# Kernel tuning notes

Hardware: AMD Instinct MI355X
Metric: run time of the kernel (lower is better)

Reference implementation:

```python
import jax, jax.numpy as jnp
import numpy as np

N_GROUPS = 32  # getGroupSize(.) assumed -> channels // 8 (or //24 for 3*ch) == 32 for ch=256
HEADS = 4


def group_norm(x, gamma, beta, groups=N_GROUPS, eps=1e-5):
    n, c = x.shape
    xg = x.reshape(n, groups, c // groups)
    mu = xg.mean(-1, keepdims=True)
    var = xg.var(-1, keepdims=True)
    xn = ((xg - mu) * jax.lax.rsqrt(var + eps)).reshape(n, c)
    return xn * gamma + beta


def setup_inputs():
    key = jax.random.key(0)
    N, E, CH, HID = 2000, 16000, 256, 256
    ks = jax.random.split(key, 24)

    def w(k, shape, s=0.02):
        return (jax.random.normal(k, shape) * s).astype(jnp.float32)

    inp = {
        'x': jax.random.normal(ks[0], (N, CH), jnp.float32),
        'edge_index': jax.random.randint(ks[1], (2, E), 0, N),
        'edge_attr': jax.random.normal(ks[2], (E, CH), jnp.float32),
        # edge_mlp: GN(3ch)+ReLU -> Linear(3ch,hid) -> GN(hid)+ReLU -> Linear(hid,ch)
        'gn_e1_g': jnp.ones((3 * CH,), jnp.float32), 'gn_e1_b': jnp.zeros((3 * CH,), jnp.float32),
        'We1': w(ks[3], (3 * CH, HID)), 'be1': jnp.zeros((HID,), jnp.float32),
        'gn_e2_g': jnp.ones((HID,), jnp.float32), 'gn_e2_b': jnp.zeros((HID,), jnp.float32),
        'We2': w(ks[4], (HID, CH)), 'be2': jnp.zeros((CH,), jnp.float32),
        # actN: GN(ch)+ReLU
        'gn_n_g': jnp.ones((CH,), jnp.float32), 'gn_n_b': jnp.zeros((CH,), jnp.float32),
        # multi-head attention projections
        'Wq': w(ks[5], (CH, CH)), 'bq': jnp.zeros((CH,), jnp.float32),
        'Wk': w(ks[6], (CH, CH)), 'bk': jnp.zeros((CH,), jnp.float32),
        'Wv': w(ks[7], (CH, CH)), 'bv': jnp.zeros((CH,), jnp.float32),
        'Wo': w(ks[8], (CH, CH)), 'bo': jnp.zeros((CH,), jnp.float32),
        # node_mlp: Linear(2ch,hid) -> GN(hid)+ReLU -> Linear(hid,ch)
        'Wn1': w(ks[9], (2 * CH, HID)), 'bn1': jnp.zeros((HID,), jnp.float32),
        'gn_n2_g': jnp.ones((HID,), jnp.float32), 'gn_n2_b': jnp.zeros((HID,), jnp.float32),
        'Wn2': w(ks[10], (HID, CH)), 'bn2': jnp.zeros((CH,), jnp.float32),
    }
    return inp


def reference(x, edge_index, edge_attr,
              gn_e1_g, gn_e1_b, We1, be1, gn_e2_g, gn_e2_b, We2, be2,
              gn_n_g, gn_n_b, Wq, bq, Wk, bk, Wv, bv, Wo, bo,
              Wn1, bn1, gn_n2_g, gn_n2_b, Wn2, bn2):
    row, col = edge_index[0], edge_index[1]
    N, ch = x.shape
    E = edge_attr.shape[0]
    dk = ch // HEADS

    # ---- edge model: cat(src, tgt, e) -> GN/ReLU -> Lin -> GN/ReLU -> Lin (+res) ----
    e_in = jnp.concatenate([x[row], x[col], edge_attr], axis=1)  # [E, 3ch]
    h = jax.nn.relu(group_norm(e_in, gn_e1_g, gn_e1_b))
    h = h @ We1 + be1
    h = jax.nn.relu(group_norm(h, gn_e2_g, gn_e2_b))
    e_out = h @ We2 + be2 + edge_attr  # [E, ch]

    # ---- node model: dense-masked MHA, queries=nodes, keys/values=edges ----
    mask = jnp.zeros((N, E), x.dtype).at[col, jnp.arange(E)].set(1.0)  # scatter adjacency
    q = (x @ Wq + bq).reshape(N, HEADS, dk)
    k = (e_out @ Wk + bk).reshape(E, HEADS, dk)
    v = (e_out @ Wv + bv).reshape(E, HEADS, dk)
    scores = jnp.einsum('nhd,ehd->hne', q, k) / jnp.sqrt(jnp.float32(dk))  # [H, N, E]
    scores = jnp.where(mask[None] > 0, scores, jnp.float32(-1e9))
    attn = jax.nn.softmax(scores, axis=-1)
    g = jnp.einsum('hne,ehd->nhd', attn, v).reshape(N, ch) @ Wo + bo  # [N, ch]

    xa = jax.nn.relu(group_norm(x, gn_n_g, gn_n_b))
    h = jnp.concatenate([xa, g], axis=1) @ Wn1 + bn1  # thinker='cat'
    h = jax.nn.relu(group_norm(h, gn_n2_g, gn_n2_b))
    n_out = h @ Wn2 + bn2 + x  # residual

    return n_out, e_out
```

## Files before the change

kernel.cpp:

```cpp
#include <hip/hip_runtime.h>
#include <hip/hip_bf16.h>
#include <stdint.h>
#include <math.h>

#define CH 256

typedef __attribute__((ext_vector_type(8)))  short short8;
typedef __attribute__((ext_vector_type(16))) short short16;
typedef __attribute__((ext_vector_type(4)))  float f32x4;

#define GL2LDS16(g, l) __builtin_amdgcn_global_load_lds(                       \
    (const __attribute__((address_space(1))) void*)(g),                        \
    (__attribute__((address_space(3))) void*)(l), 16, 0, 0)

__device__ inline short f2bf(float f) {
    __hip_bfloat16 h = __float2bfloat16(f);
    short s;
    __builtin_memcpy(&s, &h, 2);
    return s;
}

__device__ inline float bf2f(short s) {
    unsigned u = ((unsigned)(unsigned short)s) << 16;
    float f;
    __builtin_memcpy(&f, &u, 4);
    return f;
}

__device__ inline float warp_sum64(float v) {
    v += __shfl_xor(v, 32, 64);
    v += __shfl_xor(v, 16, 64);
    v += __shfl_xor(v, 8, 64);
    v += __shfl_xor(v, 4, 64);
    v += __shfl_xor(v, 2, 64);
    v += __shfl_xor(v, 1, 64);
    return v;
}

__device__ inline float warp_max64(float v) {
    v = fmaxf(v, __shfl_xor(v, 32, 64));
    v = fmaxf(v, __shfl_xor(v, 16, 64));
    v = fmaxf(v, __shfl_xor(v, 8, 64));
    v = fmaxf(v, __shfl_xor(v, 4, 64));
    v = fmaxf(v, __shfl_xor(v, 2, 64));
    v = fmaxf(v, __shfl_xor(v, 1, 64));
    return v;
}

struct GArgs {
    const short* A; const short* Bt; const float* bias; const float* res;
    float* C; short* Cbf;
    const float* gamma; const float* beta; float* vbar;
    int M, K, Nc, ldc, coff;
    const short* A2; const short* Bt2; const float* bias2; short* Cbf2;
    int M2, Nc2, y_split;
    const short* xbf; const short* eabf; const int* rowi; const int* coli;
    const float* mu; const float* rs; const float* vg; const float* vbt;
};

template <int BM, int BN, int AMODE, int EPI, int DUAL, int VB>
__global__ __launch_bounds__(256) void mfma_gemm(GArgs g)
{
    constexpr int BK = 64;
    constexpr int AK = AMODE ? (BK + 8) : BK;
    constexpr int HM = BM / 2, HN = BN / 2;
    constexpr int FM = HM / 16, FN = HN / 16;
    constexpr int PA = BM / 32;
    constexpr int PB = BN / 32;
    __shared__ short As[BM * AK];
    __shared__ short Bs[BN * BK];
    __shared__ int sidx[AMODE ? 2 * BM : 1];

    const short* A = g.A; const short* Bt = g.Bt;
    const float* bias = g.bias; const float* res = g.res;
    float* C = g.C; short* Cbf = g.Cbf;
    int M = g.M, ldc = g.ldc, co = g.coff;
    const int K = g.K;
    int by = blockIdx.y, bx = blockIdx.x;
    bool qrole = false;
    if constexpr (DUAL) {
        if (by >= g.y_split) {
            by -= g.y_split;
            if (bx * BN >= g.Nc2) return;
            qrole = true;
            A = g.A2; Bt = g.Bt2; bias = g.bias2; Cbf = g.Cbf2;
            C = nullptr; res = nullptr;
            M = g.M2; ldc = g.Nc2; co = 0;
        }
    }

    const int t = threadIdx.x;
    const int wave = t >> 6, lane = t & 63;
    const int q = lane >> 4, l16 = lane & 15;
    const int row0 = by * BM;
    const int col0 = bx * BN;
    const int wm = wave & 1, wn = wave >> 1;

    if constexpr (AMODE) {
        if (t < BM) {
            int gr = row0 + t; if (gr >= M) gr = M - 1;
            sidx[t] = g.rowi[gr];
            sidx[BM + t] = g.coli[gr];
        }
        __syncthreads();
    }

    f32x4 acc[FM][FN];
    #pragma unroll
    for (int i = 0; i < FM; i++)
        #pragma unroll
        for (int j = 0; j < FN; j++) acc[i][j] = (f32x4){0.f, 0.f, 0.f, 0.f};

    for (int k0 = 0; k0 < K; k0 += BK) {
        if constexpr (AMODE == 1) {
            int reg = k0 >> 8;
            int rloc = t >> 3;
            int c8 = (t & 7) * 8;
            int pos = k0 + c8;
            int G = pos / 24;
            float4 ga  = *(const float4*)&g.vg[pos];
            float4 ga2 = *(const float4*)&g.vg[pos + 4];
            float4 gb  = *(const float4*)&g.vbt[pos];
            float4 gb2 = *(const float4*)&g.vbt[pos + 4];
            int off = pos & 255;
            #pragma unroll
            for (int p = 0; p < BM / 32; p++) {
                int r2 = p * 32 + rloc;
                int e = row0 + r2; if (e >= M) e = M - 1;
                const short* srow;
                if (reg == 0)      srow = g.xbf + (size_t)sidx[r2] * CH;
                else if (reg == 1) srow = g.xbf + (size_t)sidx[BM + r2] * CH;
                else               srow = g.eabf + (size_t)e * CH;
                short8 v8 = *(const short8*)&srow[off];
                float mm = g.mu[(size_t)e * 32 + G];
                float rr = g.rs[(size_t)e * 32 + G];
                short8 o;
                o[0] = f2bf(fmaxf((bf2f(v8[0]) - mm) * rr * ga.x + gb.x, 0.f));
                o[1] = f2bf(fmaxf((bf2f(v8[1]) - mm) * rr * ga.y + gb.y, 0.f));
                o[2] = f2bf(fmaxf((bf2f(v8[2]) - mm) * rr * ga.z + gb.z, 0.f));
                o[3] = f2bf(fmaxf((bf2f(v8[3]) - mm) * rr * ga.w + gb.w, 0.f));
                o[4] = f2bf(fmaxf((bf2f(v8[4]) - mm) * rr * ga2.x + gb2.x, 0.f));
                o[5] = f2bf(fmaxf((bf2f(v8[5]) - mm) * rr * ga2.y + gb2.y, 0.f));
                o[6] = f2bf(fmaxf((bf2f(v8[6]) - mm) * rr * ga2.z + gb2.z, 0.f));
                o[7] = f2bf(fmaxf((bf2f(v8[7]) - mm) * rr * ga2.w + gb2.w, 0.f));
                *(short8*)&As[r2 * AK + c8] = o;
            }
        } else {
            #pragma unroll
            for (int p = 0; p < PA; p++) {
                int chunk = p * 256 + t;
                int r = chunk >> 3;
                int cs = (((chunk & 7) ^ (r & 7)) * 8);
                int gr = row0 + r; if (gr >= M) gr = M - 1;
                const short* gsrc = A + (size_t)gr * K + k0 + cs;
                short* ldst = &As[(p * 256 + wave * 64) * 8];
                GL2LDS16(gsrc, ldst);
            }
        }
        #pragma unroll
        for (int p = 0; p < PB; p++) {
            int chunk = p * 256 + t;
            int r = chunk >> 3;
            int cs = (((chunk & 7) ^ (r & 7)) * 8);
            const short* gsrc = Bt + (size_t)(col0 + r) * K + k0 + cs;
            short* ldst = &Bs[(p * 256 + wave * 64) * 8];
            GL2LDS16(gsrc, ldst);
        }
        __syncthreads();
        #pragma unroll
        for (int ks = 0; ks < 2; ks++) {
            short8 af[FM], bf[FN];
            #pragma unroll
            for (int mi = 0; mi < FM; mi++) {
                int R = wm * HM + mi * 16 + l16;
                if constexpr (AMODE == 1)
                    af[mi] = *(const short8*)&As[R * AK + ks * 32 + q * 8];
                else {
                    int slot = ((ks * 4 + q) ^ (R & 7)) * 8;
                    af[mi] = *(const short8*)&As[R * BK + slot];
                }
            }
            #pragma unroll
            for (int ni = 0; ni < FN; ni++) {
                int R = wn * HN + ni * 16 + l16;
                int slot = ((ks * 4 + q) ^ (R & 7)) * 8;
                bf[ni] = *(const short8*)&Bs[R * BK + slot];
            }
            #pragma unroll
            for (int mi = 0; mi < FM; mi++)
                #pragma unroll
                for (int ni = 0; ni < FN; ni++)
                    acc[mi][ni] = __builtin_amdgcn_mfma_f32_16x16x32_bf16(
                        af[mi], bf[ni], acc[mi][ni], 0, 0, 0);
        }
        __syncthreads();
    }

    #pragma unroll
    for (int ni = 0; ni < FN; ni++) {
        int cg = col0 + wn * HN + ni * 16 + l16;
        float bv = bias[cg];
        if constexpr (EPI == 1) {
            float ga = g.gamma[cg], be = g.beta[cg];
            #pragma unroll
            for (int mi = 0; mi < FM; mi++) {
                #pragma unroll
                for (int r = 0; r < 4; r++) {
                    float v = acc[mi][ni][r] + bv;
                    float s = v, sq = v * v;
                    s += __shfl_xor(s, 1, 64);  sq += __shfl_xor(sq, 1, 64);
                    s += __shfl_xor(s, 2, 64);  sq += __shfl_xor(sq, 2, 64);
                    s += __shfl_xor(s, 4, 64);  sq += __shfl_xor(sq, 4, 64);
                    float mean = s * 0.125f;
                    float var = sq * 0.125f - mean * mean;
                    float o = fmaxf((v - mean) * rsqrtf(var + 1e-5f) * ga + be, 0.f);
                    int rg = row0 + wm * HM + mi * 16 + q * 4 + r;
                    if (rg < M) Cbf[(size_t)rg * ldc + co + cg] = f2bf(o);
                }
            }
        } else {
            #pragma unroll
            for (int mi = 0; mi < FM; mi++) {
                #pragma unroll
                for (int r = 0; r < 4; r++) {
                    int rg = row0 + wm * HM + mi * 16 + q * 4 + r;
                    if (rg < M) {
                        float v = acc[mi][ni][r] + bv;
                        if (res) v += res[(size_t)rg * ldc + co + cg];
                        if (C)   C[(size_t)rg * ldc + co + cg] = v;
                        if (Cbf) Cbf[(size_t)rg * ldc + co + cg] = f2bf(v);
                    }
                }
            }
            if constexpr (VB) {
                if (!qrole && cg >= 256) {
                    float part = 0.f;
                    #pragma unroll
                    for (int mi = 0; mi < FM; mi++)
                        #pragma unroll
                        for (int r = 0; r < 4; r++) {
                            int rg = row0 + wm * HM + mi * 16 + q * 4 + r;
                            if (rg < M) part += acc[mi][ni][r] + bv;
                        }
                    part += __shfl_xor(part, 16, 64);
                    part += __shfl_xor(part, 32, 64);
                    if (q == 0) atomicAdd(&g.vbar[cg - 256], part);
                }
            }
        }
    }
}

struct PrepPack {
    const float* wsrc[8];
    short* wdst[8];
    int wK[8];
    int wstart[8];
    int NW, NP;
    const float* x;
    short* x_bf;
    short* cat_bf;
    float2* xs;
    const float* gng;
    const float* gnb;
    float* vbar;
    const float* bk;
    const float* bv;
    float* bkv;
    int* counts;
    int N;
};

__global__ __launch_bounds__(256) void prep_kernel(PrepPack p)
{
    int bid = blockIdx.x;
    int t = threadIdx.x;
    if (bid < p.NW) {
        int m = 0;
        #pragma unroll
        for (int i = 1; i < 8; i++) if (bid >= p.wstart[i]) m = i;
        int k0 = (bid - p.wstart[m]) * 16;
        const float* src = p.wsrc[m];
        short16 o;
        #pragma unroll
        for (int j = 0; j < 16; j++) o[j] = f2bf(src[(size_t)(k0 + j) * 256 + t]);
        *(short16*)(p.wdst[m] + (size_t)t * p.wK[m] + k0) = o;
        return;
    }
    if (bid >= p.NW + p.NP) {
        int i = (bid - p.NW - p.NP) * 256 + t;
        if (i < p.N) p.counts[i] = 0;
        return;
    }
    int pb = bid - p.NW;
    if (pb == 0) {
        p.vbar[t] = 0.f;
        p.bkv[t] = p.bk[t];
        p.bkv[256 + t] = p.bv[t];
    }
    int r = pb * 8 + (t >> 5);
    int g = t & 31;
    if (r >= p.N) return;
    size_t xb = (size_t)r * CH + g * 8;
    float4 a = *(const float4*)&p.x[xb];
    float4 b = *(const float4*)&p.x[xb + 4];
    short8 xr;
    xr[0] = f2bf(a.x); xr[1] = f2bf(a.y); xr[2] = f2bf(a.z); xr[3] = f2bf(a.w);
    xr[4] = f2bf(b.x); xr[5] = f2bf(b.y); xr[6] = f2bf(b.z); xr[7] = f2bf(b.w);
    *(short8*)&p.x_bf[xb] = xr;
    float s  = a.x + a.y + a.z + a.w + b.x + b.y + b.z + b.w;
    float s2 = a.x*a.x + a.y*a.y + a.z*a.z + a.w*a.w
             + b.x*b.x + b.y*b.y + b.z*b.z + b.w*b.w;
    p.xs[(size_t)r * 32 + g] = make_float2(s, s2);
    float m = s * 0.125f;
    float var = s2 * 0.125f - m * m;
    float rsd = rsqrtf(var + 1e-5f);
    float4 g0 = *(const float4*)&p.gng[g * 8];
    float4 g1 = *(const float4*)&p.gng[g * 8 + 4];
    float4 b0 = *(const float4*)&p.gnb[g * 8];
    float4 b1 = *(const float4*)&p.gnb[g * 8 + 4];
    short8 o;
    o[0] = f2bf(fmaxf((a.x - m) * rsd * g0.x + b0.x, 0.f));
    o[1] = f2bf(fmaxf((a.y - m) * rsd * g0.y + b0.y, 0.f));
    o[2] = f2bf(fmaxf((a.z - m) * rsd * g0.z + b0.z, 0.f));
    o[3] = f2bf(fmaxf((a.w - m) * rsd * g0.w + b0.w, 0.f));
    o[4] = f2bf(fmaxf((b.x - m) * rsd * g1.x + b1.x, 0.f));
    o[5] = f2bf(fmaxf((b.y - m) * rsd * g1.y + b1.y, 0.f));
    o[6] = f2bf(fmaxf((b.z - m) * rsd * g1.z + b1.z, 0.f));
    o[7] = f2bf(fmaxf((b.w - m) * rsd * g1.w + b1.w, 0.f));
    *(short8*)&p.cat_bf[(size_t)r * (2 * CH) + g * 8] = o;
}

__global__ __launch_bounds__(256) void estats_kernel(
    const float* __restrict__ eattr, const int* __restrict__ rowi,
    const int* __restrict__ coli, const float2* __restrict__ xs,
    float* __restrict__ mu, float* __restrict__ rs,
    short* __restrict__ eabf, int* __restrict__ counts, int E)
{
    __shared__ float2 ea[8][32];
    int t = threadIdx.x;
    int slot = t >> 5, g = t & 31;
    int e = blockIdx.x * 8 + slot;
    float4 a = *(const float4*)&eattr[(size_t)e * CH + g * 8];
    float4 b = *(const float4*)&eattr[(size_t)e * CH + g * 8 + 4];
    short8 o8;
    o8[0] = f2bf(a.x); o8[1] = f2bf(a.y); o8[2] = f2bf(a.z); o8[3] = f2bf(a.w);
    o8[4] = f2bf(b.x); o8[5] = f2bf(b.y); o8[6] = f2bf(b.z); o8[7] = f2bf(b.w);
    *(short8*)&eabf[(size_t)e * CH + g * 8] = o8;
    float s  = a.x + a.y + a.z + a.w + b.x + b.y + b.z + b.w;
    float s2 = a.x*a.x + a.y*a.y + a.z*a.z + a.w*a.w
             + b.x*b.x + b.y*b.y + b.z*b.z + b.w*b.w;
    ea[slot][g] = make_float2(s, s2);
    int r = rowi[e], c = coli[e];
    if (g == 0) atomicAdd(&counts[c], 1);
    __syncthreads();
    float S = 0.f, S2 = 0.f;
    #pragma unroll
    for (int j = 0; j < 3; j++) {
        int b3 = 3 * g + j;
        int src = b3 >> 5, idx = b3 & 31;
        float2 v;
        if (src == 0)      v = xs[(size_t)r * 32 + idx];
        else if (src == 1) v = xs[(size_t)c * 32 + idx];
        else               v = ea[slot][idx];
        S += v.x; S2 += v.y;
    }
    float m = S * (1.f / 24.f);
    float var = S2 * (1.f / 24.f) - m * m;
    mu[(size_t)e * 32 + g] = m;
    rs[(size_t)e * 32 + g] = rsqrtf(var + 1e-5f);
}

__global__ __launch_bounds__(1024) void scan_kernel(
    const int* __restrict__ counts, int* __restrict__ offsets,
    int* __restrict__ cursor, int N)
{
    __shared__ int s[1024];
    int t = threadIdx.x;
    int a = (2 * t     < N) ? counts[2 * t]     : 0;
    int b = (2 * t + 1 < N) ? counts[2 * t + 1] : 0;
    s[t] = a + b;
    __syncthreads();
    for (int off = 1; off < 1024; off <<= 1) {
        int v = (t >= off) ? s[t - off] : 0;
        __syncthreads();
        s[t] += v;
        __syncthreads();
    }
    int excl = (t > 0) ? s[t - 1] : 0;
    if (2 * t < N)     { offsets[2 * t]     = excl;     cursor[2 * t]     = excl; }
    if (2 * t + 1 < N) { offsets[2 * t + 1] = excl + a; cursor[2 * t + 1] = excl + a; }
    if (t == 1023) offsets[N] = s[1023];
}

__global__ __launch_bounds__(256) void escore_kernel(
    const short* __restrict__ qb, const short* __restrict__ kvb,
    const int* __restrict__ coli, int* __restrict__ cursor,
    int* __restrict__ elist, float* __restrict__ sc, int E)
{
    int e = blockIdx.x * 4 + (threadIdx.x >> 6);
    int lane = threadIdx.x & 63;
    if (e >= E) return;
    int c = coli[e];
    if (lane == 0) { int p = atomicAdd(&cursor[c], 1); elist[p] = e; }
    const short* qrow = qb + (size_t)c * CH;
    const short* krow = kvb + (size_t)e * 512;
    float d0 = bf2f(qrow[lane])       * bf2f(krow[lane]);
    float d1 = bf2f(qrow[64 + lane])  * bf2f(krow[64 + lane]);
    float d2 = bf2f(qrow[128 + lane]) * bf2f(krow[128 + lane]);
    float d3 = bf2f(qrow[192 + lane]) * bf2f(krow[192 + lane]);
    d0 = warp_sum64(d0);
    d1 = warp_sum64(d1);
    d2 = warp_sum64(d2);
    d3 = warp_sum64(d3);
    if (lane == 0) {
        float4 o = {d0 * 0.125f, d1 * 0.125f, d2 * 0.125f, d3 * 0.125f};
        *(float4*)&sc[(size_t)e * 4] = o;
    }
}

__global__ __launch_bounds__(256) void attn_kernel(
    const float* __restrict__ sc, const short* __restrict__ kvb,
    const int* __restrict__ offsets, const int* __restrict__ elist,
    const float* __restrict__ vbar, short* __restrict__ g_bf, int N, int E)
{
    int n = blockIdx.x;
    int h = threadIdx.x >> 6;
    int lane = threadIdx.x & 63;
    int s0 = offsets[n], s1 = offsets[n + 1];
    float out = 0.f;
    if (s1 > s0) {
        float m = -INFINITY, l = 0.f;
        for (int base = s0; base < s1; base += 64) {
            int cn = s1 - base; if (cn > 64) cn = 64;
            int e = (lane < cn) ? elist[base + lane] : 0;
            float s = (lane < cn) ? sc[(size_t)e * 4 + h] : -INFINITY;
            float mc = warp_max64(s);
            float nm = fmaxf(m, mc);
            float scale = __expf(m - nm);
            float pp = (lane < cn) ? __expf(s - nm) : 0.f;
            float ps = warp_sum64(pp);
            l = l * scale + ps;
            out *= scale;
            m = nm;
            for (int i = 0; i < cn; i++) {
                float pi = __shfl(pp, i, 64);
                int   ei = __shfl(e, i, 64);
                out += pi * bf2f(kvb[(size_t)ei * 512 + 256 + h * 64 + lane]);
            }
        }
        out /= l;
    } else {
        out = vbar[h * 64 + lane] * (1.f / (float)E);
    }
    g_bf[(size_t)n * CH + h * 64 + lane] = f2bf(out);
}

extern "C" void kernel_launch(void* const* d_in, const int* in_sizes, int n_in,
                              void* d_out, int out_size, void* d_ws, size_t ws_size,
                              hipStream_t stream)
{
    const float* x       = (const float*)d_in[0];
    const int*   ei      = (const int*)d_in[1];
    const float* eattr   = (const float*)d_in[2];
    const float* gn_e1_g = (const float*)d_in[3];
    const float* gn_e1_b = (const float*)d_in[4];
    const float* We1     = (const float*)d_in[5];
    const float* be1     = (const float*)d_in[6];
    const float* gn_e2_g = (const float*)d_in[7];
    const float* gn_e2_b = (const float*)d_in[8];
    const float* We2     = (const float*)d_in[9];
    const float* be2     = (const float*)d_in[10];
    const float* gn_n_g  = (const float*)d_in[11];
    const float* gn_n_b  = (const float*)d_in[12];
    const float* Wq      = (const float*)d_in[13];
    const float* bq      = (const float*)d_in[14];
    const float* Wk      = (const float*)d_in[15];
    const float* bk      = (const float*)d_in[16];
    const float* Wv      = (const float*)d_in[17];
    const float* bv      = (const float*)d_in[18];
    const float* Wo      = (const float*)d_in[19];
    const float* bo      = (const float*)d_in[20];
    const float* Wn1     = (const float*)d_in[21];
    const float* bn1     = (const float*)d_in[22];
    const float* gn_n2_g = (const float*)d_in[23];
    const float* gn_n2_b = (const float*)d_in[24];
    const float* Wn2     = (const float*)d_in[25];
    const float* bn2     = (const float*)d_in[26];

    const int N = in_sizes[0] / CH;
    const int E = in_sizes[2] / CH;

    float* nout = (float*)d_out;
    float* eout = (float*)d_out + (size_t)N * CH;

    char* base = (char*)d_ws;
    short* kv_bf  = (short*)base; base += (size_t)E * 512 * 2;
    short* h2_bf  = (short*)base; base += (size_t)E * CH * 2;
    short* eo_bf  = (short*)base; base += (size_t)E * CH * 2;
    short* eabf   = (short*)base; base += (size_t)E * CH * 2;
    short* q_bf   = (short*)base; base += (size_t)N * CH * 2;
    short* g_bf   = (short*)base; base += (size_t)N * CH * 2;
    short* cat_bf = (short*)base; base += (size_t)N * 2 * CH * 2;
    short* hn_bf  = (short*)base; base += (size_t)N * CH * 2;
    short* x_bf   = (short*)base; base += (size_t)N * CH * 2;
    float2* xs    = (float2*)base; base += (size_t)N * 32 * 8;
    float* mub    = (float*)base; base += (size_t)E * 32 * 4;
    float* rsb    = (float*)base; base += (size_t)E * 32 * 4;
    float* sc     = (float*)base; base += (size_t)E * 4 * 4;
    float* vbar   = (float*)base; base += 1024;
    float* bkv    = (float*)base; base += 2048;
    short* We1t = (short*)base; base += (size_t)768 * 256 * 2;
    short* We2t = (short*)base; base += (size_t)256 * 256 * 2;
    short* Wqt  = (short*)base; base += (size_t)256 * 256 * 2;
    short* Wkvt = (short*)base; base += (size_t)512 * 256 * 2;
    short* Wot  = (short*)base; base += (size_t)256 * 256 * 2;
    short* Wn1t = (short*)base; base += (size_t)512 * 256 * 2;
    short* Wn2t = (short*)base; base += (size_t)256 * 256 * 2;
    int* counts  = (int*)base;
    int* offsets = counts + N;
    int* cursor  = offsets + (N + 1) + 3;
    int* elist   = cursor + N;

    const int* rowi = ei;
    const int* coli = ei + E;

    dim3 blk(256);

    PrepPack pp;
    const float* wsrc[8] = {We1, We2, Wq, Wk, Wv, Wo, Wn1, Wn2};
    short* wdst[8] = {We1t, We2t, Wqt, Wkvt, Wkvt + (size_t)256 * 256, Wot, Wn1t, Wn2t};
    const int wKd[8] = {768, 256, 256, 256, 256, 256, 512, 256};
    int acc = 0;
    for (int i = 0; i < 8; i++) {
        pp.wsrc[i] = wsrc[i]; pp.wdst[i] = wdst[i]; pp.wK[i] = wKd[i];
        pp.wstart[i] = acc; acc += wKd[i] / 16;
    }
    pp.NW = acc;
    pp.NP = (N + 7) / 8;
    pp.x = x; pp.x_bf = x_bf; pp.cat_bf = cat_bf; pp.xs = xs;
    pp.gng = gn_n_g; pp.gnb = gn_n_b;
    pp.vbar = vbar; pp.bk = bk; pp.bv = bv; pp.bkv = bkv;
    pp.counts = counts; pp.N = N;
    int nzero = (N + 255) / 256;
    prep_kernel<<<pp.NW + pp.NP + nzero, blk, 0, stream>>>(pp);

    estats_kernel<<<E / 8, blk, 0, stream>>>(eattr, rowi, coli, xs, mub, rsb,
                                             eabf, counts, E);
    scan_kernel<<<1, 1024, 0, stream>>>(counts, offsets, cursor, N);

    GArgs ga = {};
    ga.Bt = We1t; ga.bias = be1; ga.Cbf = h2_bf;
    ga.gamma = gn_e2_g; ga.beta = gn_e2_b;
    ga.M = E; ga.K = 3 * CH; ga.Nc = CH; ga.ldc = CH; ga.coff = 0;
    ga.xbf = x_bf; ga.eabf = eabf; ga.rowi = rowi; ga.coli = coli;
    ga.mu = mub; ga.rs = rsb; ga.vg = gn_e1_g; ga.vbt = gn_e1_b;
    mfma_gemm<64, 128, 1, 1, 0, 0><<<dim3(2, E / 64), blk, 0, stream>>>(ga);

    ga = {};
    ga.A = h2_bf; ga.Bt = We2t; ga.bias = be2; ga.res = eattr;
    ga.C = eout; ga.Cbf = eo_bf;
    ga.M = E; ga.K = CH; ga.Nc = CH; ga.ldc = CH; ga.coff = 0;
    mfma_gemm<64, 128, 0, 0, 0, 0><<<dim3(2, E / 64), blk, 0, stream>>>(ga);

    ga = {};
    ga.A = eo_bf; ga.Bt = Wkvt; ga.bias = bkv; ga.Cbf = kv_bf; ga.vbar = vbar;
    ga.M = E; ga.K = CH; ga.Nc = 512; ga.ldc = 512; ga.coff = 0;
    ga.A2 = x_bf; ga.Bt2 = Wqt; ga.bias2 = bq; ga.Cbf2 = q_bf;
    ga.M2 = N; ga.Nc2 = CH; ga.y_split = E / 64;
    mfma_gemm<64, 128, 0, 0, 1, 1><<<dim3(4, E / 64 + (N + 63) / 64), blk, 0, stream>>>(ga);

    escore_kernel<<<(E + 3) / 4, blk, 0, stream>>>(q_bf, kv_bf, coli, cursor, elist, sc, E);
    attn_kernel<<<N, blk, 0, stream>>>(sc, kv_bf, offsets, elist, vbar, g_bf, N, E);

    ga = {};
    ga.A = g_bf; ga.Bt = Wot; ga.bias = bo; ga.Cbf = cat_bf;
    ga.M = N; ga.K = CH; ga.Nc = CH; ga.ldc = 2 * CH; ga.coff = CH;
    mfma_gemm<32, 64, 0, 0, 0, 0><<<dim3(4, (N + 31) / 32), blk, 0, stream>>>(ga);

    ga = {};
    ga.A = cat_bf; ga.Bt = Wn1t; ga.bias = bn1; ga.Cbf = hn_bf;
    ga.gamma = gn_n2_g; ga.beta = gn_n2_b;
    ga.M = N; ga.K = 2 * CH; ga.Nc = CH; ga.ldc = CH; ga.coff = 0;
    mfma_gemm<32, 64, 0, 1, 0, 0><<<dim3(4, (N + 31) / 32), blk, 0, stream>>>(ga);

    ga = {};
    ga.A = hn_bf; ga.Bt = Wn2t; ga.bias = bn2; ga.res = x; ga.C = nout;
    ga.M = N; ga.K = CH; ga.Nc = CH; ga.ldc = CH; ga.coff = 0;
    mfma_gemm<32, 64, 0, 0, 0, 0><<<dim3(4, (N + 31) / 32), blk, 0, stream>>>(ga);
}
```

Measured before the change: 248.2 us.

## Fuse edge MLP and K/V/Q projections into one mega edge kernel

Replaces the three edge-side GEMM launches (We1 with fused GroupNorm input, We2 with residual, and the dual KV/Q projection) with a single kernel. Each block handles 32 edges across the full 256-wide output and keeps the intermediate hidden and e_out tiles in LDS, so the h2 and eo bf16 round-trips through global memory disappear. Extra blocks at the end of the grid compute the Q projection. The trade-off is smaller row tiles, full-width B staging with no overlap between loads and MFMAs, and larger LDS use per block, which may lower occupancy and weight reuse.

Result: slower. 258.2 us (+4.0%).

```diff
diff --git a/kernel.cpp b/kernel.cpp
--- a/kernel.cpp
+++ b/kernel.cpp
@@ -47,122 +47,267 @@
     return v;
 }
 
-struct GArgs {
-    const short* A; const short* Bt; const float* bias; const float* res;
-    float* C; short* Cbf;
-    const float* gamma; const float* beta; float* vbar;
-    int M, K, Nc, ldc, coff;
-    const short* A2; const short* Bt2; const float* bias2; short* Cbf2;
-    int M2, Nc2, y_split;
+struct MArgs {
     const short* xbf; const short* eabf; const int* rowi; const int* coli;
-    const float* mu; const float* rs; const float* vg; const float* vbt;
+    const float* mu; const float* rs;
+    const float* vg; const float* vbt;
+    const short* We1t; const float* be1;
+    const float* g2; const float* b2;
+    const short* We2t; const float* be2;
+    const float* eattr; float* eout;
+    const short* Wkvt; const float* bkv; short* kvbf; float* vbar;
+    int E, EB;
+    const short* Wqt; const float* bq; short* qbf; int N;
 };
 
-template <int BM, int BN, int AMODE, int EPI, int DUAL, int VB>
-__global__ __launch_bounds__(256) void mfma_gemm(GArgs g)
+__global__ __launch_bounds__(256) void mega_edge(MArgs a)
 {
-    constexpr int BK = 64;
-    constexpr int AK = AMODE ? (BK + 8) : BK;
-    constexpr int HM = BM / 2, HN = BN / 2;
-    constexpr int FM = HM / 16, FN = HN / 16;
-    constexpr int PA = BM / 32;
-    constexpr int PB = BN / 32;
-    __shared__ short As[BM * AK];
-    __shared__ short Bs[BN * BK];
-    __shared__ int sidx[AMODE ? 2 * BM : 1];
-
-    const short* A = g.A; const short* Bt = g.Bt;
-    const float* bias = g.bias; const float* res = g.res;
-    float* C = g.C; short* Cbf = g.Cbf;
-    int M = g.M, ldc = g.ldc, co = g.coff;
-    const int K = g.K;
-    int by = blockIdx.y, bx = blockIdx.x;
-    bool qrole = false;
-    if constexpr (DUAL) {
-        if (by >= g.y_split) {
-            by -= g.y_split;
-            if (bx * BN >= g.Nc2) return;
-            qrole = true;
-            A = g.A2; Bt = g.Bt2; bias = g.bias2; Cbf = g.Cbf2;
-            C = nullptr; res = nullptr;
-            M = g.M2; ldc = g.Nc2; co = 0;
-        }
-    }
+    __shared__ short Bs[256 * 64];
+    __shared__ short As[32 * 72];
+    __shared__ short hs[32 * 264];
+    __shared__ int sidx[64];
 
     const int t = threadIdx.x;
     const int wave = t >> 6, lane = t & 63;
     const int q = lane >> 4, l16 = lane & 15;
-    const int row0 = by * BM;
-    const int col0 = bx * BN;
     const int wm = wave & 1, wn = wave >> 1;
-
-    if constexpr (AMODE) {
-        if (t < BM) {
-            int gr = row0 + t; if (gr >= M) gr = M - 1;
-            sidx[t] = g.rowi[gr];
-            sidx[BM + t] = g.coli[gr];
-        }
-        __syncthreads();
-    }
-
-    f32x4 acc[FM][FN];
+    const int bid = blockIdx.x;
+
+    auto stageB = [&](const short* Bt, int colbase, int Kb, int k0) {
+        #pragma unroll
+        for (int p = 0; p < 8; p++) {
+            int chunk = p * 256 + t;
+            int r = chunk >> 3;
+            int cs = ((chunk & 7) ^ (r & 7)) * 8;
+            const short* gsrc = Bt + (size_t)(colbase + r) * Kb + k0 + cs;
+            short* ldst = &Bs[(p * 256 + wave * 64) * 8];
+            GL2LDS16(gsrc, ldst);
+        }
+    };
+    auto mmaStep = [&](const short* Ab, int as, int koff, f32x4* acc) {
+        #pragma unroll
+        for (int ks = 0; ks < 2; ks++) {
+            short8 af = *(const short8*)&Ab[(wm * 16 + l16) * as + koff + ks * 32 + q * 8];
+            #pragma unroll
+            for (int ni = 0; ni < 8; ni++) {
+                int R = wn * 128 + ni * 16 + l16;
+                int slot = ((ks * 4 + q) ^ (R & 7)) * 8;
+                short8 bf = *(const short8*)&Bs[R * 64 + slot];
+                acc[ni] = __builtin_amdgcn_mfma_f32_16x16x32_bf16(af, bf, acc[ni], 0, 0, 0);
+            }
+        }
+    };
+
+    f32x4 acc[8];
+
+    if (bid >= a.EB) {
+        int row0 = (bid - a.EB) * 32;
+        #pragma unroll
+        for (int i = 0; i < 8; i++) acc[i] = (f32x4){0.f, 0.f, 0.f, 0.f};
+        for (int k0 = 0; k0 < 256; k0 += 64) {
+            {
+                int r = t >> 3;
+                int cs = ((t & 7) ^ (r & 7)) * 8;
+                int gr = row0 + r; if (gr >= a.N) gr = a.N - 1;
+                const short* gsrc = a.xbf + (size_t)gr * CH + k0 + cs;
+                short* ldst = &As[(wave * 64) * 8];
+                GL2LDS16(gsrc, ldst);
+            }
+            stageB(a.Wqt, 0, 256, k0);
+            __syncthreads();
+            #pragma unroll
+            for (int ks = 0; ks < 2; ks++) {
+                int R = wm * 16 + l16;
+                int slot = ((ks * 4 + q) ^ (R & 7)) * 8;
+                short8 af = *(const short8*)&As[R * 64 + slot];
+                #pragma unroll
+                for (int ni = 0; ni < 8; ni++) {
+                    int Rb = wn * 128 + ni * 16 + l16;
+                    int sb = ((ks * 4 + q) ^ (Rb & 7)) * 8;
+                    short8 bf = *(const short8*)&Bs[Rb * 64 + sb];
+                    acc[ni] = __builtin_amdgcn_mfma_f32_16x16x32_bf16(af, bf, acc[ni], 0, 0, 0);
+                }
+            }
+            __syncthreads();
+        }
+        #pragma unroll
+        for (int ni = 0; ni < 8; ni++) {
+            int cg = wn * 128 + ni * 16 + l16;
+            float bv = a.bq[cg];
+            #pragma unroll
+            for (int r = 0; r < 4; r++) {
+                int rg = row0 + wm * 16 + q * 4 + r;
+                if (rg < a.N) a.qbf[(size_t)rg * CH + cg] = f2bf(acc[ni][r] + bv);
+            }
+        }
+        return;
+    }
+
+    int row0 = bid * 32;
+    if (t < 32) { sidx[t] = a.rowi[row0 + t]; sidx[32 + t] = a.coli[row0 + t]; }
+    __syncthreads();
+
     #pragma unroll
-    for (int i = 0; i < FM; i++)
-        #pragma unroll
-        for (int j = 0; j < FN; j++) acc[i][j] = (f32x4){0.f, 0.f, 0.f, 0.f};
-
-    for (int k0 = 0; k0 < K; k0 += BK) {
-        if constexpr (AMODE == 1) {
+    for (int i = 0; i < 8; i++) acc[i] = (f32x4){0.f, 0.f, 0.f, 0.f};
+    for (int k0 = 0; k0 < 768; k0 += 64) {
+        {
             int reg = k0 >> 8;
             int rloc = t >> 3;
             int c8 = (t & 7) * 8;
             int pos = k0 + c8;
             int G = pos / 24;
-            float4 ga  = *(const float4*)&g.vg[pos];
-            float4 ga2 = *(const float4*)&g.vg[pos + 4];
-            float4 gb  = *(const float4*)&g.vbt[pos];
-            float4 gb2 = *(const float4*)&g.vbt[pos + 4];
+            float4 ga  = *(const float4*)&a.vg[pos];
+            float4 ga2 = *(const float4*)&a.vg[pos + 4];
+            float4 gb  = *(const float4*)&a.vbt[pos];
+            float4 gb2 = *(const float4*)&a.vbt[pos + 4];
             int off = pos & 255;
-            #pragma unroll
-            for (int p = 0; p < BM / 32; p++) {
-                int r2 = p * 32 + rloc;
-                int e = row0 + r2; if (e >= M) e = M - 1;
-                const short* srow;
-                if (reg == 0)      srow = g.xbf + (size_t)sidx[r2] * CH;
-                else if (reg == 1) srow = g.xbf + (size_t)sidx[BM + r2] * CH;
-                else               srow = g.eabf + (size_t)e * CH;
-                short8 v8 = *(const short8*)&srow[off];
-                float mm = g.mu[(size_t)e * 32 + G];
-                float rr = g.rs[(size_t)e * 32 + G];
-                short8 o;
-                o[0] = f2bf(fmaxf((bf2f(v8[0]) - mm) * rr * ga.x + gb.x, 0.f));
-                o[1] = f2bf(fmaxf((bf2f(v8[1]) - mm) * rr * ga.y + gb.y, 0.f));
-                o[2] = f2bf(fmaxf((bf2f(v8[2]) - mm) * rr * ga.z + gb.z, 0.f));
-                o[3] = f2bf(fmaxf((bf2f(v8[3]) - mm) * rr * ga.w + gb.w, 0.f));
-                o[4] = f2bf(fmaxf((bf2f(v8[4]) - mm) * rr * ga2.x + gb2.x, 0.f));
-                o[5] = f2bf(fmaxf((bf2f(v8[5]) - mm) * rr * ga2.y + gb2.y, 0.f));
-                o[6] = f2bf(fmaxf((bf2f(v8[6]) - mm) * rr * ga2.z + gb2.z, 0.f));
-                o[7] = f2bf(fmaxf((bf2f(v8[7]) - mm) * rr * ga2.w + gb2.w, 0.f));
-                *(short8*)&As[r2 * AK + c8] = o;
-            }
-        } else {
-            #pragma unroll
-            for (int p = 0; p < PA; p++) {
-                int chunk = p * 256 + t;
-                int r = chunk >> 3;
-                int cs = (((chunk & 7) ^ (r & 7)) * 8);
-                int gr = row0 + r; if (gr >= M) gr = M - 1;
-                const short* gsrc = A + (size_t)gr * K + k0 + cs;
-                short* ldst = &As[(p * 256 + wave * 64) * 8];
-                GL2LDS16(gsrc, ldst);
-            }
+            int e = row0 + rloc;
+            const short* srow;
+            if (reg == 0)      srow = a.xbf + (size_t)sidx[rloc] * CH;
+            else if (reg == 1) srow = a.xbf + (size_t)sidx[32 + rloc] * CH;
+            else               srow = a.eabf + (size_t)e * CH;
+            short8 v8 = *(const short8*)&srow[off];
+            float mm = a.mu[(size_t)e * 32 + G];
+            float rr = a.rs[(size_t)e * 32 + G];
+            short8 o;
+            o[0] = f2bf(fmaxf((bf2f(v8[0]) - mm) * rr * ga.x + gb.x, 0.f));
+            o[1] = f2bf(fmaxf((bf2f(v8[1]) - mm) * rr * ga.y + gb.y, 0.f));
+            o[2] = f2bf(fmaxf((bf2f(v8[2]) - mm) * rr * ga.z + gb.z, 0.f));
+            o[3] = f2bf(fmaxf((bf2f(v8[3]) - mm) * rr * ga.w + gb.w, 0.f));
+            o[4] = f2bf(fmaxf((bf2f(v8[4]) - mm) * rr * ga2.x + gb2.x, 0.f));
+            o[5] = f2bf(fmaxf((bf2f(v8[5]) - mm) * rr * ga2.y + gb2.y, 0.f));
+            o[6] = f2bf(fmaxf((bf2f(v8[6]) - mm) * rr * ga2.z + gb2.z, 0.f));
+            o[7] = f2bf(fmaxf((bf2f(v8[7]) - mm) * rr * ga2.w + gb2.w, 0.f));
+            *(short8*)&As[rloc * 72 + c8] = o;
+        }
+        stageB(a.We1t, 0, 768, k0);
+        __syncthreads();
+        mmaStep(As, 72, 0, acc);
+        __syncthreads();
+    }
+    #pragma unroll
+    for (int ni = 0; ni < 8; ni++) {
+        int cg = wn * 128 + ni * 16 + l16;
+        float bv = a.be1[cg];
+        float ga = a.g2[cg], be = a.b2[cg];
+        #pragma unroll
+        for (int r = 0; r < 4; r++) {
+            float v = acc[ni][r] + bv;
+            float s = v, sq = v * v;
+            s += __shfl_xor(s, 1, 64);  sq += __shfl_xor(sq, 1, 64);
+            s += __shfl_xor(s, 2, 64);  sq += __shfl_xor(sq, 2, 64);
+            s += __shfl_xor(s, 4, 64);  sq += __shfl_xor(sq, 4, 64);
+            float mean = s * 0.125f;
+            float var = sq * 0.125f - mean * mean;
+            float o = fmaxf((v - mean) * rsqrtf(var + 1e-5f) * ga + be, 0.f);
+            int rl = wm * 16 + q * 4 + r;
+            hs[rl * 264 + cg] = f2bf(o);
+        }
+    }
+    __syncthreads();
+
+    #pragma unroll
+    for (int i = 0; i < 8; i++) acc[i] = (f32x4){0.f, 0.f, 0.f, 0.f};
+    for (int k0 = 0; k0 < 256; k0 += 64) {
+        stageB(a.We2t, 0, 256, k0);
+        __syncthreads();
+        mmaStep(hs, 264, k0, acc);
+        __syncthreads();
+    }
+    #pragma unroll
+    for (int ni = 0; ni < 8; ni++) {
+        int cg = wn * 128 + ni * 16 + l16;
+        float bv = a.be2[cg];
+        #pragma unroll
+        for (int r = 0; r < 4; r++) {
+            int rl = wm * 16 + q * 4 + r;
+            int rg = row0 + rl;
+            float v = acc[ni][r] + bv + a.eattr[(size_t)rg * CH + cg];
+            a.eout[(size_t)rg * CH + cg] = v;
+            hs[rl * 264 + cg] = f2bf(v);
+        }
+    }
+    __syncthreads();
+
+    #pragma unroll
+    for (int half = 0; half < 2; half++) {
+        #pragma unroll
+        for (int i = 0; i < 8; i++) acc[i] = (f32x4){0.f, 0.f, 0.f, 0.f};
+        for (int k0 = 0; k0 < 256; k0 += 64) {
+            stageB(a.Wkvt, half * 256, 256, k0);
+            __syncthreads();
+            mmaStep(hs, 264, k0, acc);
+            __syncthreads();
+        }
+        #pragma unroll
+        for (int ni = 0; ni < 8; ni++) {
+            int cg = wn * 128 + ni * 16 + l16;
+            float bv = a.bkv[half * 256 + cg];
+            float part = 0.f;
+            #pragma unroll
+            for (int r = 0; r < 4; r++) {
+                int rg = row0 + wm * 16 + q * 4 + r;
+                float v = acc[ni][r] + bv;
+                a.kvbf[(size_t)rg * 512 + half * 256 + cg] = f2bf(v);
+                part += v;
+            }
+            if (half == 1) {
+                part += __shfl_xor(part, 16, 64);
+                part += __shfl_xor(part, 32, 64);
+                if (q == 0) atomicAdd(&a.vbar[cg], part);
+            }
+        }
+    }
+}
+
+struct GArgs {
+    const short* A; const short* Bt; const float* bias; const float* res;
+    float* C; short* Cbf;
+    const float* gamma; const float* beta;
+    int M, K, Nc, ldc, coff;
+};
+
+template <int BM, int BN, int EPI>
+__global__ __launch_bounds__(256) void mfma_gemm(GArgs g)
+{
+    constexpr int BK = 64;
+    constexpr int HM = BM / 2, HN = BN / 2;
+    constexpr int FM = HM / 16, FN = HN / 16;
+    constexpr int PA = BM / 32;
+    constexpr int PB = BN / 32;
+    __shared__ short As[BM * BK];
+    __shared__ short Bs[BN * BK];
+
+    const int t = threadIdx.x;
+    const int wave = t >> 6, lane = t & 63;
+    const int q = lane >> 4, l16 = lane & 15;
+    const int row0 = blockIdx.y * BM;
+    const int col0 = blockIdx.x * BN;
+    const int wm = wave & 1, wn = wave >> 1;
+
+    f32x4 acc[FM][FN];
+    #pragma unroll
+    for (int i = 0; i < FM; i++)
+        #pragma unroll
+        for (int j = 0; j < FN; j++) acc[i][j] = (f32x4){0.f, 0.f, 0.f, 0.f};
+
+    for (int k0 = 0; k0 < g.K; k0 += BK) {
+        #pragma unroll
+        for (int p = 0; p < PA; p++) {
+            int chunk = p * 256 + t;
+            int r = chunk >> 3;
+            int cs = (((chunk & 7) ^ (r & 7)) * 8);
+            int gr = row0 + r; if (gr >= g.M) gr = g.M - 1;
+            const short* gsrc = g.A + (size_t)gr * g.K + k0 + cs;
+            short* ldst = &As[(p * 256 + wave * 64) * 8];
+            GL2LDS16(gsrc, ldst);
         }
         #pragma unroll
         for (int p = 0; p < PB; p++) {
             int chunk = p * 256 + t;
             int r = chunk >> 3;
             int cs = (((chunk & 7) ^ (r & 7)) * 8);
-            const short* gsrc = Bt + (size_t)(col0 + r) * K + k0 + cs;
+            const short* gsrc = g.Bt + (size_t)(col0 + r) * g.K + k0 + cs;
             short* ldst = &Bs[(p * 256 + wave * 64) * 8];
             GL2LDS16(gsrc, ldst);
         }
@@ -173,12 +318,8 @@
             #pragma unroll
             for (int mi = 0; mi < FM; mi++) {
                 int R = wm * HM + mi * 16 + l16;
-                if constexpr (AMODE == 1)
-                    af[mi] = *(const short8*)&As[R * AK + ks * 32 + q * 8];
-                else {
-                    int slot = ((ks * 4 + q) ^ (R & 7)) * 8;
-                    af[mi] = *(const short8*)&As[R * BK + slot];
-                }
+                int slot = ((ks * 4 + q) ^ (R & 7)) * 8;
+                af[mi] = *(const short8*)&As[R * BK + slot];
             }
             #pragma unroll
             for (int ni = 0; ni < FN; ni++) {
@@ -199,7 +340,7 @@
     #pragma unroll
     for (int ni = 0; ni < FN; ni++) {
         int cg = col0 + wn * HN + ni * 16 + l16;
-        float bv = bias[cg];
+        float bv = g.bias[cg];
         if constexpr (EPI == 1) {
             float ga = g.gamma[cg], be = g.beta[cg];
             #pragma unroll
@@ -215,7 +356,7 @@
                     float var = sq * 0.125f - mean * mean;
                     float o = fmaxf((v - mean) * rsqrtf(var + 1e-5f) * ga + be, 0.f);
                     int rg = row0 + wm * HM + mi * 16 + q * 4 + r;
-                    if (rg < M) Cbf[(size_t)rg * ldc + co + cg] = f2bf(o);
+                    if (rg < g.M) g.Cbf[(size_t)rg * g.ldc + g.coff + cg] = f2bf(o);
                 }
             }
         } else {
@@ -224,27 +365,12 @@
                 #pragma unroll
                 for (int r = 0; r < 4; r++) {
                     int rg = row0 + wm * HM + mi * 16 + q * 4 + r;
-                    if (rg < M) {
+                    if (rg < g.M) {
                         float v = acc[mi][ni][r] + bv;
-                        if (res) v += res[(size_t)rg * ldc + co + cg];
-                        if (C)   C[(size_t)rg * ldc + co + cg] = v;
-                        if (Cbf) Cbf[(size_t)rg * ldc + co + cg] = f2bf(v);
+                        if (g.res) v += g.res[(size_t)rg * g.ldc + g.coff + cg];
+                        if (g.C)   g.C[(size_t)rg * g.ldc + g.coff + cg] = v;
+                        if (g.Cbf) g.Cbf[(size_t)rg * g.ldc + g.coff + cg] = f2bf(v);
                     }
-                }
-            }
-            if constexpr (VB) {
-                if (!qrole && cg >= 256) {
-                    float part = 0.f;
-                    #pragma unroll
-                    for (int mi = 0; mi < FM; mi++)
-                        #pragma unroll
-                        for (int r = 0; r < 4; r++) {
-                            int rg = row0 + wm * HM + mi * 16 + q * 4 + r;
-                            if (rg < M) part += acc[mi][ni][r] + bv;
-                        }
-                    part += __shfl_xor(part, 16, 64);
-                    part += __shfl_xor(part, 32, 64);
-                    if (q == 0) atomicAdd(&g.vbar[cg - 256], part);
                 }
             }
         }
@@ -496,8 +622,6 @@
 
     char* base = (char*)d_ws;
     short* kv_bf  = (short*)base; base += (size_t)E * 512 * 2;
-    short* h2_bf  = (short*)base; base += (size_t)E * CH * 2;
-    short* eo_bf  = (short*)base; base += (size_t)E * CH * 2;
     short* eabf   = (short*)base; base += (size_t)E * CH * 2;
     short* q_bf   = (short*)base; base += (size_t)N * CH * 2;
     short* g_bf   = (short*)base; base += (size_t)N * CH * 2;
@@ -549,43 +673,35 @@
                                              eabf, counts, E);
     scan_kernel<<<1, 1024, 0, stream>>>(counts, offsets, cursor, N);
 
-    GArgs ga = {};
-    ga.Bt = We1t; ga.bias = be1; ga.Cbf = h2_bf;
-    ga.gamma = gn_e2_g; ga.beta = gn_e2_b;
-    ga.M = E; ga.K = 3 * CH; ga.Nc = CH; ga.ldc = CH; ga.coff = 0;
-    ga.xbf = x_bf; ga.eabf = eabf; ga.rowi = rowi; ga.coli = coli;
-    ga.mu = mub; ga.rs = rsb; ga.vg = gn_e1_g; ga.vbt = gn_e1_b;
-    mfma_gemm<64, 128, 1, 1, 0, 0><<<dim3(2, E / 64), blk, 0, stream>>>(ga);
-
-    ga = {};
-    ga.A = h2_bf; ga.Bt = We2t; ga.bias = be2; ga.res = eattr;
-    ga.C = eout; ga.Cbf = eo_bf;
-    ga.M = E; ga.K = CH; ga.Nc = CH; ga.ldc = CH; ga.coff = 0;
-    mfma_gemm<64, 128, 0, 0, 0, 0><<<dim3(2, E / 64), blk, 0, stream>>>(ga);
-
-    ga = {};
-    ga.A = eo_bf; ga.Bt = Wkvt; ga.bias = bkv; ga.Cbf = kv_bf; ga.vbar = vbar;
-    ga.M = E; ga.K = CH; ga.Nc = 512; ga.ldc = 512; ga.coff = 0;
-    ga.A2 = x_bf; ga.Bt2 = Wqt; ga.bias2 = bq; ga.Cbf2 = q_bf;
-    ga.M2 = N; ga.Nc2 = CH; ga.y_split = E / 64;
-    mfma_gemm<64, 128, 0, 0, 1, 1><<<dim3(4, E / 64 + (N + 63) / 64), blk, 0, stream>>>(ga);
+    MArgs ma;
+    ma.xbf = x_bf; ma.eabf = eabf; ma.rowi = rowi; ma.coli = coli;
+    ma.mu = mub; ma.rs = rsb;
+    ma.vg = gn_e1_g; ma.vbt = gn_e1_b;
+    ma.We1t = We1t; ma.be1 = be1;
+    ma.g2 = gn_e2_g; ma.b2 = gn_e2_b;
+    ma.We2t = We2t; ma.be2 = be2;
+    ma.eattr = eattr; ma.eout = eout;
+    ma.Wkvt = Wkvt; ma.bkv = bkv; ma.kvbf = kv_bf; ma.vbar = vbar;
+    ma.E = E; ma.EB = E / 32;
+    ma.Wqt = Wqt; ma.bq = bq; ma.qbf = q_bf; ma.N = N;
+    mega_edge<<<E / 32 + (N + 31) / 32, blk, 0, stream>>>(ma);
 
     escore_kernel<<<(E + 3) / 4, blk, 0, stream>>>(q_bf, kv_bf, coli, cursor, elist, sc, E);
     attn_kernel<<<N, blk, 0, stream>>>(sc, kv_bf, offsets, elist, vbar, g_bf, N, E);
 
-    ga = {};
+    GArgs ga = {};
     ga.A = g_bf; ga.Bt = Wot; ga.bias = bo; ga.Cbf = cat_bf;
     ga.M = N; ga.K = CH; ga.Nc = CH; ga.ldc = 2 * CH; ga.coff = CH;
-    mfma_gemm<32, 64, 0, 0, 0, 0><<<dim3(4, (N + 31) / 32), blk, 0, stream>>>(ga);
+    mfma_gemm<32, 64, 0><<<dim3(4, (N + 31) / 32), blk, 0, stream>>>(ga);
 
     ga = {};
     ga.A = cat_bf; ga.Bt = Wn1t; ga.bias = bn1; ga.Cbf = hn_bf;
     ga.gamma = gn_n2_g; ga.beta = gn_n2_b;
     ga.M = N; ga.K = 2 * CH; ga.Nc = CH; ga.ldc = CH; ga.coff = 0;
-    mfma_gemm<32, 64, 0, 1, 0, 0><<<dim3(4, (N + 31) / 32), blk, 0, stream>>>(ga);
+    mfma_gemm<32, 64, 1><<<dim3(4, (N + 31) / 32), blk, 0, stream>>>(ga);
 
     ga = {};
     ga.A = hn_bf; ga.Bt = Wn2t; ga.bias = bn2; ga.res = x; ga.C = nout;
     ga.M = N; ga.K = CH; ga.Nc = CH; ga.ldc = CH; ga.coff = 0;
-    mfma_gemm<32, 64, 0, 0, 0, 0><<<dim3(4, (N + 31) / 32), blk, 0, stream>>>(ga);
-}
+    mfma_gemm<32, 64, 0><<<dim3(4, (N + 31) / 32), blk, 0, stream>>>(ga);
+}
```

## Fuse edge scoring into attention kernel and move elist fill into KV GEMM

Applied to the files above, without the earlier changes.

Removes the separate per-edge score kernel. Each attention block now computes its q·k dot products for its edges into shared memory before the online softmax. Building the CSR edge list by atomics moves into the KV/Q projection GEMM (one column block per row tile), which also saves a launch and the score buffer round trip. The edge GEMMs also drop from BN=128 to BN=64 with twice the column blocks, which gives more parallelism but reloads the A tiles more often.

Measured after the change: 238.0 us. 1.04x faster.

```diff
diff --git a/kernel.cpp b/kernel.cpp
--- a/kernel.cpp
+++ b/kernel.cpp
@@ -56,9 +56,10 @@
     int M2, Nc2, y_split;
     const short* xbf; const short* eabf; const int* rowi; const int* coli;
     const float* mu; const float* rs; const float* vg; const float* vbt;
+    int* cursor; int* elist;
 };
 
-template <int BM, int BN, int AMODE, int EPI, int DUAL, int VB>
+template <int BM, int BN, int AMODE, int EPI, int DUAL, int VB, int FILL>
 __global__ __launch_bounds__(256) void mfma_gemm(GArgs g)
 {
     constexpr int BK = 64;
@@ -103,6 +104,17 @@
             sidx[BM + t] = g.coli[gr];
         }
         __syncthreads();
+    }
+
+    if constexpr (FILL) {
+        if (!qrole && bx == 0 && t < BM) {
+            int rg = row0 + t;
+            if (rg < M) {
+                int c = g.coli[rg];
+                int p = atomicAdd(&g.cursor[c], 1);
+                g.elist[p] = rg;
+            }
+        }
     }
 
     f32x4 acc[FM][FN];
@@ -393,67 +405,61 @@
     if (t == 1023) offsets[N] = s[1023];
 }
 
-__global__ __launch_bounds__(256) void escore_kernel(
+__global__ __launch_bounds__(256) void attn_kernel(
     const short* __restrict__ qb, const short* __restrict__ kvb,
-    const int* __restrict__ coli, int* __restrict__ cursor,
-    int* __restrict__ elist, float* __restrict__ sc, int E)
-{
-    int e = blockIdx.x * 4 + (threadIdx.x >> 6);
-    int lane = threadIdx.x & 63;
-    if (e >= E) return;
-    int c = coli[e];
-    if (lane == 0) { int p = atomicAdd(&cursor[c], 1); elist[p] = e; }
-    const short* qrow = qb + (size_t)c * CH;
-    const short* krow = kvb + (size_t)e * 512;
-    float d0 = bf2f(qrow[lane])       * bf2f(krow[lane]);
-    float d1 = bf2f(qrow[64 + lane])  * bf2f(krow[64 + lane]);
-    float d2 = bf2f(qrow[128 + lane]) * bf2f(krow[128 + lane]);
-    float d3 = bf2f(qrow[192 + lane]) * bf2f(krow[192 + lane]);
-    d0 = warp_sum64(d0);
-    d1 = warp_sum64(d1);
-    d2 = warp_sum64(d2);
-    d3 = warp_sum64(d3);
-    if (lane == 0) {
-        float4 o = {d0 * 0.125f, d1 * 0.125f, d2 * 0.125f, d3 * 0.125f};
-        *(float4*)&sc[(size_t)e * 4] = o;
-    }
-}
-
-__global__ __launch_bounds__(256) void attn_kernel(
-    const float* __restrict__ sc, const short* __restrict__ kvb,
     const int* __restrict__ offsets, const int* __restrict__ elist,
     const float* __restrict__ vbar, short* __restrict__ g_bf, int N, int E)
 {
+    __shared__ int eidx[64];
+    __shared__ float scl[4 * 64];
     int n = blockIdx.x;
-    int h = threadIdx.x >> 6;
+    int wave = threadIdx.x >> 6;
     int lane = threadIdx.x & 63;
     int s0 = offsets[n], s1 = offsets[n + 1];
-    float out = 0.f;
-    if (s1 > s0) {
-        float m = -INFINITY, l = 0.f;
-        for (int base = s0; base < s1; base += 64) {
-            int cn = s1 - base; if (cn > 64) cn = 64;
-            int e = (lane < cn) ? elist[base + lane] : 0;
-            float s = (lane < cn) ? sc[(size_t)e * 4 + h] : -INFINITY;
-            float mc = warp_max64(s);
-            float nm = fmaxf(m, mc);
-            float scale = __expf(m - nm);
-            float pp = (lane < cn) ? __expf(s - nm) : 0.f;
-            float ps = warp_sum64(pp);
-            l = l * scale + ps;
-            out *= scale;
-            m = nm;
-            for (int i = 0; i < cn; i++) {
-                float pi = __shfl(pp, i, 64);
-                int   ei = __shfl(e, i, 64);
-                out += pi * bf2f(kvb[(size_t)ei * 512 + 256 + h * 64 + lane]);
-            }
-        }
-        out /= l;
-    } else {
-        out = vbar[h * 64 + lane] * (1.f / (float)E);
-    }
-    g_bf[(size_t)n * CH + h * 64 + lane] = f2bf(out);
+    float q0 = bf2f(qb[(size_t)n * CH + lane]);
+    float q1 = bf2f(qb[(size_t)n * CH + 64 + lane]);
+    float q2 = bf2f(qb[(size_t)n * CH + 128 + lane]);
+    float q3 = bf2f(qb[(size_t)n * CH + 192 + lane]);
+    float out = 0.f, m = -INFINITY, l = 0.f;
+    for (int base = s0; base < s1; base += 64) {
+        int cn = s1 - base; if (cn > 64) cn = 64;
+        if (wave == 0 && lane < cn) eidx[lane] = elist[base + lane];
+        __syncthreads();
+        for (int j = wave; j < cn; j += 4) {
+            int e = eidx[j];
+            const short* kr = kvb + (size_t)e * 512;
+            float d0 = warp_sum64(q0 * bf2f(kr[lane]));
+            float d1 = warp_sum64(q1 * bf2f(kr[64 + lane]));
+            float d2 = warp_sum64(q2 * bf2f(kr[128 + lane]));
+            float d3 = warp_sum64(q3 * bf2f(kr[192 + lane]));
+            if (lane == 0) {
+                scl[j]       = d0 * 0.125f;
+                scl[64 + j]  = d1 * 0.125f;
+                scl[128 + j] = d2 * 0.125f;
+                scl[192 + j] = d3 * 0.125f;
+            }
+        }
+        __syncthreads();
+        float s = (lane < cn) ? scl[wave * 64 + lane] : -INFINITY;
+        float mc = warp_max64(s);
+        float nm = fmaxf(m, mc);
+        float scale = __expf(m - nm);
+        float pp = (lane < cn) ? __expf(s - nm) : 0.f;
+        float ps = warp_sum64(pp);
+        l = l * scale + ps;
+        out *= scale;
+        m = nm;
+        for (int i = 0; i < cn; i++) {
+            float pi = __shfl(pp, i, 64);
+            int ei = eidx[i];
+            out += pi * bf2f(kvb[(size_t)ei * 512 + 256 + wave * 64 + lane]);
+        }
+        __syncthreads();
+    }
+    float res;
+    if (s1 > s0) res = out / l;
+    else         res = vbar[wave * 64 + lane] * (1.f / (float)E);
+    g_bf[(size_t)n * CH + wave * 64 + lane] = f2bf(res);
 }
 
 extern "C" void kernel_launch(void* const* d_in, const int* in_sizes, int n_in,
@@ -507,7 +513,6 @@
     float2* xs    = (float2*)base; base += (size_t)N * 32 * 8;
     float* mub    = (float*)base; base += (size_t)E * 32 * 4;
     float* rsb    = (float*)base; base += (size_t)E * 32 * 4;
-    float* sc     = (float*)base; base += (size_t)E * 4 * 4;
     float* vbar   = (float*)base; base += 1024;
     float* bkv    = (float*)base; base += 2048;
     short* We1t = (short*)base; base += (size_t)768 * 256 * 2;
@@ -555,37 +560,37 @@
     ga.M = E; ga.K = 3 * CH; ga.Nc = CH; ga.ldc = CH; ga.coff = 0;
     ga.xbf = x_bf; ga.eabf = eabf; ga.rowi = rowi; ga.coli = coli;
     ga.mu = mub; ga.rs = rsb; ga.vg = gn_e1_g; ga.vbt = gn_e1_b;
-    mfma_gemm<64, 128, 1, 1, 0, 0><<<dim3(2, E / 64), blk, 0, stream>>>(ga);
+    mfma_gemm<64, 64, 1, 1, 0, 0, 0><<<dim3(4, E / 64), blk, 0, stream>>>(ga);
 
     ga = {};
     ga.A = h2_bf; ga.Bt = We2t; ga.bias = be2; ga.res = eattr;
     ga.C = eout; ga.Cbf = eo_bf;
     ga.M = E; ga.K = CH; ga.Nc = CH; ga.ldc = CH; ga.coff = 0;
-    mfma_gemm<64, 128, 0, 0, 0, 0><<<dim3(2, E / 64), blk, 0, stream>>>(ga);
+    mfma_gemm<64, 64, 0, 0, 0, 0, 0><<<dim3(4, E / 64), blk, 0, stream>>>(ga);
 
     ga = {};
     ga.A = eo_bf; ga.Bt = Wkvt; ga.bias = bkv; ga.Cbf = kv_bf; ga.vbar = vbar;
     ga.M = E; ga.K = CH; ga.Nc = 512; ga.ldc = 512; ga.coff = 0;
     ga.A2 = x_bf; ga.Bt2 = Wqt; ga.bias2 = bq; ga.Cbf2 = q_bf;
     ga.M2 = N; ga.Nc2 = CH; ga.y_split = E / 64;
-    mfma_gemm<64, 128, 0, 0, 1, 1><<<dim3(4, E / 64 + (N + 63) / 64), blk, 0, stream>>>(ga);
-
-    escore_kernel<<<(E + 3) / 4, blk, 0, stream>>>(q_bf, kv_bf, coli, cursor, elist, sc, E);
-    attn_kernel<<<N, blk, 0, stream>>>(sc, kv_bf, offsets, elist, vbar, g_bf, N, E);
+    ga.coli = coli; ga.cursor = cursor; ga.elist = elist;
+    mfma_gemm<64, 64, 0, 0, 1, 1, 1><<<dim3(8, E / 64 + (N + 63) / 64), blk, 0, stream>>>(ga);
+
+    attn_kernel<<<N, blk, 0, stream>>>(q_bf, kv_bf, offsets, elist, vbar, g_bf, N, E);
 
     ga = {};
     ga.A = g_bf; ga.Bt = Wot; ga.bias = bo; ga.Cbf = cat_bf;
     ga.M = N; ga.K = CH; ga.Nc = CH; ga.ldc = 2 * CH; ga.coff = CH;
-    mfma_gemm<32, 64, 0, 0, 0, 0><<<dim3(4, (N + 31) / 32), blk, 0, stream>>>(ga);
+    mfma_gemm<32, 64, 0, 0, 0, 0, 0><<<dim3(4, (N + 31) / 32), blk, 0, stream>>>(ga);
 
     ga = {};
     ga.A = cat_bf; ga.Bt = Wn1t; ga.bias = bn1; ga.Cbf = hn_bf;
     ga.gamma = gn_n2_g; ga.beta = gn_n2_b;
     ga.M = N; ga.K = 2 * CH; ga.Nc = CH; ga.ldc = CH; ga.coff = 0;
-    mfma_gemm<32, 64, 0, 1, 0, 0><<<dim3(4, (N + 31) / 32), blk, 0, stream>>>(ga);
+    mfma_gemm<32, 64, 0, 1, 0, 0, 0><<<dim3(4, (N + 31) / 32), blk, 0, stream>>>(ga);
 
     ga = {};
     ga.A = hn_bf; ga.Bt = Wn2t; ga.bias = bn2; ga.res = x; ga.C = nout;
     ga.M = N; ga.K = CH; ga.Nc = CH; ga.ldc = CH; ga.coff = 0;
-    mfma_gemm<32, 64, 0, 0, 0, 0><<<dim3(4, (N + 31) / 32), blk, 0, stream>>>(ga);
-}
+    mfma_gemm<32, 64, 0, 0, 0, 0, 0><<<dim3(4, (N + 31) / 32), blk, 0, stream>>>(ga);
+}
```
